# Kernel optimization log

Measured on AMD Instinct MI355X. Metric: run time of the kernel, lower is better.

## Reference

```python
import jax, jax.numpy as jnp
import numpy as np

N = 16384      # nodes (256 chess boards x 64 squares)
E = 393216     # edges (avg degree 24)
G = 256        # graphs
HID = 128
H = 4
C = 32         # head dim
L = 8          # 4 blocks x 2 GATv2Conv
NODE_DIM = 21
EDGE_DIM = 6


def setup_inputs() -> dict:
    key = jax.random.key(0)
    ks = jax.random.split(key, 12)
    x = jax.random.normal(ks[0], (N, NODE_DIM), jnp.float32)
    edge_index = jax.random.randint(ks[1], (2, E), 0, N, dtype=jnp.int32)
    edge_attr = jax.random.uniform(ks[2], (E, EDGE_DIM), dtype=jnp.float32)
    batch = jnp.sort(jax.random.randint(ks[3], (N,), 0, G, dtype=jnp.int32))

    def w(k, shape, fan_in):
        return jax.random.normal(k, shape, jnp.float32) * (1.0 / np.sqrt(fan_in))

    Win = w(ks[4], (NODE_DIM, HID), NODE_DIM)
    b_in = jnp.zeros((HID,), jnp.float32)
    Wl = w(ks[5], (L, HID, HID), HID)
    bl = jnp.zeros((L, HID), jnp.float32)
    Wr = w(ks[6], (L, HID, HID), HID)
    br = jnp.zeros((L, HID), jnp.float32)
    We = w(ks[7], (L, EDGE_DIM, HID), EDGE_DIM)
    att = w(ks[8], (L, H, C), C)
    bconv = jnp.zeros((L, HID), jnp.float32)
    gamma = jnp.ones((L, HID), jnp.float32)
    beta = jnp.zeros((L, HID), jnp.float32)
    W1 = w(ks[9], (HID, 64), HID)
    b1 = jnp.zeros((64,), jnp.float32)
    W2 = w(ks[10], (64, 3), 64)
    b2 = jnp.zeros((3,), jnp.float32)
    return dict(x=x, edge_index=edge_index, edge_attr=edge_attr, batch=batch,
                Win=Win, b_in=b_in, Wl=Wl, bl=bl, Wr=Wr, br=br, We=We, att=att,
                bconv=bconv, gamma=gamma, beta=beta, W1=W1, b1=b1, W2=W2, b2=b2)


def _gatv2(h, src, dst, ea, Wl, bl, Wr, br, We, att, bias):
    # PyG GATv2Conv: message j->i uses x_j from lin_l, x_i from lin_r
    xl = (h @ Wl + bl).reshape(N, H, C)
    xr = (h @ Wr + br).reshape(N, H, C)
    ee = (ea @ We).reshape(-1, H, C)
    m = jax.nn.leaky_relu(xl[src] + xr[dst] + ee, 0.2)   # [Ef, H, C]
    s = jnp.einsum('ehc,hc->eh', m, att)                 # [Ef, H]
    smax = jax.ops.segment_max(s, dst, num_segments=N)   # self-loops => no empty segs
    ex = jnp.exp(s - smax[dst])
    den = jax.ops.segment_sum(ex, dst, num_segments=N)
    alpha = ex / den[dst]                                # edge softmax per target node
    out = jax.ops.segment_sum(alpha[:, :, None] * xl[src], dst, num_segments=N)
    return out.reshape(N, HID) + bias


def _bn(x, g, b):
    mu = jnp.mean(x, axis=0)
    var = jnp.var(x, axis=0)
    return g * (x - mu) * jax.lax.rsqrt(var + 1e-5) + b


def reference(x, edge_index, edge_attr, batch, Win, b_in, Wl, bl, Wr, br, We, att,
              bconv, gamma, beta, W1, b1, W2, b2):
    src0, dst0 = edge_index[0], edge_index[1]
    # add self-loops with fill_value='mean' (per-target mean of incoming edge_attr)
    deg = jax.ops.segment_sum(jnp.ones((E,), jnp.float32), dst0, num_segments=N)
    loop_attr = jax.ops.segment_sum(edge_attr, dst0, num_segments=N) / jnp.maximum(deg, 1.0)[:, None]
    idx = jnp.arange(N, dtype=src0.dtype)
    src = jnp.concatenate([src0, idx])
    dst = jnp.concatenate([dst0, idx])
    ea = jnp.concatenate([edge_attr, loop_attr], axis=0)

    h = jax.nn.relu(x @ Win + b_in)
    for blk in range(4):
        res = h
        l = 2 * blk
        h = jax.nn.relu(_bn(_gatv2(h, src, dst, ea, Wl[l], bl[l], Wr[l], br[l], We[l], att[l], bconv[l]), gamma[l], beta[l]))
        l = 2 * blk + 1
        h = _bn(_gatv2(h, src, dst, ea, Wl[l], bl[l], Wr[l], br[l], We[l], att[l], bconv[l]), gamma[l], beta[l])
        h = jax.nn.relu(h + res)

    cnt = jnp.maximum(jax.ops.segment_sum(jnp.ones((N,), jnp.float32), batch, num_segments=G), 1.0)
    pooled = jax.ops.segment_sum(h, batch, num_segments=G) / cnt[:, None]
    logits = jax.nn.relu(pooled @ W1 + b1) @ W2 + b2
    return logits
```

## Files before the change

### kernel.cpp

```cpp
#include <hip/hip_runtime.h>
#include <hip/hip_fp16.h>
#include <math.h>

constexpr int N   = 16384;
constexpr int E   = 393216;
constexpr int G   = 256;
constexpr int HID = 128;
constexpr int SLOT = 64;

__device__ __forceinline__ float red16(float x) {
    union fi { float f; int i; };
    fi a, b;
    a.f = x;
    b.i = __builtin_amdgcn_mov_dpp(a.i, 0x121, 0xf, 0xf, false); a.f += b.f;
    b.i = __builtin_amdgcn_mov_dpp(a.i, 0x122, 0xf, 0xf, false); a.f += b.f;
    b.i = __builtin_amdgcn_mov_dpp(a.i, 0x124, 0xf, 0xf, false); a.f += b.f;
    b.i = __builtin_amdgcn_mov_dpp(a.i, 0x128, 0xf, 0xf, false); a.f += b.f;
    return a.f;
}

__global__ __launch_bounds__(256) void k_scatter(const int* __restrict__ src,
                                                 const int* __restrict__ dst,
                                                 int* __restrict__ fill,
                                                 const float* __restrict__ edge_attr,
                                                 int* __restrict__ csr_src,
                                                 float* __restrict__ csr_ea) {
    int e = blockIdx.x * 256 + threadIdx.x;
    if (e >= E) return;
    int d = dst[e];
    int pos = atomicAdd(&fill[d], 1);
    if (pos > 62) return;
    size_t base = (size_t)d * SLOT + pos;
    csr_src[base] = src[e];
    const float* s = edge_attr + (size_t)e * 6;
    float4 a = {s[0], s[1], s[2], s[3]};
    float4 b = {s[4], s[5], 0.0f, 0.0f};
    float4* dstp = (float4*)(csr_ea + base * 8);
    dstp[0] = a;
    dstp[1] = b;
}

__global__ __launch_bounds__(256) void k_loopattr2(const int* __restrict__ fill,
                                                   int* __restrict__ csr_src,
                                                   float* __restrict__ csr_ea) {
    int i = blockIdx.x * 256 + threadIdx.x;
    if (i >= N) return;
    int deg = fill[i];
    deg = deg > 62 ? 62 : deg;
    size_t e0 = (size_t)i * SLOT;
    float4 sa = {0, 0, 0, 0};
    float sbx = 0.0f, sby = 0.0f;
    for (int e = 0; e < deg; e++) {
        const float4* p = (const float4*)(csr_ea + (e0 + e) * 8);
        float4 a = p[0];
        float4 b = p[1];
        sa.x += a.x; sa.y += a.y; sa.z += a.z; sa.w += a.w;
        sbx += b.x; sby += b.y;
    }
    float inv = 1.0f / fmaxf((float)deg, 1.0f);
    float4 oa = {sa.x * inv, sa.y * inv, sa.z * inv, sa.w * inv};
    float4 ob = {sbx * inv, sby * inv, 0.0f, 0.0f};
    float4* q = (float4*)(csr_ea + (e0 + deg) * 8);
    q[0] = oa;
    q[1] = ob;
    csr_src[e0 + deg] = i;
}

__global__ __launch_bounds__(128) void k_ingemm(const float* __restrict__ x,
                                                const float* __restrict__ Win,
                                                const float* __restrict__ b_in,
                                                float* __restrict__ h) {
    __shared__ float xs[21];
    int i = blockIdx.x;
    int c = threadIdx.x;
    if (c < 21) xs[c] = x[i * 21 + c];
    __syncthreads();
    float acc = b_in[c];
#pragma unroll
    for (int d = 0; d < 21; d++) acc += xs[d] * Win[d * HID + c];
    h[i * HID + c] = fmaxf(acc, 0.0f);
}

__global__ __launch_bounds__(256) void k_gemm_lr(const float* __restrict__ h,
                                                 const float* __restrict__ bns,
                                                 const float* __restrict__ gamma,
                                                 const float* __restrict__ beta,
                                                 float* __restrict__ res,
                                                 const float* __restrict__ Wl,
                                                 const float* __restrict__ bl,
                                                 const float* __restrict__ Wr,
                                                 const float* __restrict__ br,
                                                 __half2* __restrict__ XLh,
                                                 float* __restrict__ XR) {
    __shared__ float hs[16][HID];
    __shared__ float sc[HID], sh[HID];
    int t = threadIdx.x;
    int r0 = blockIdx.x * 16;
    if (bns) {
        if (t < 128) {
            const float invN = 1.0f / (float)N;
            float mean = bns[t] * invN;
            float var  = bns[128 + t] * invN - mean * mean;
            float inv  = rsqrtf(var + 1e-5f);
            float s = gamma[t] * inv;
            sc[t] = s;
            sh[t] = beta[t] - mean * s;
        }
        __syncthreads();
    }
    {
        int row = t >> 4;
        int col = (t & 15) * 8;
        size_t base = (size_t)(r0 + row) * HID + col;
        const float4* src = (const float4*)&h[base];
        float4 a = src[0];
        float4 b = src[1];
        if (bns) {
            float4 s0 = *(const float4*)&sc[col];
            float4 s1 = *(const float4*)&sc[col + 4];
            float4 h0 = *(const float4*)&sh[col];
            float4 h1 = *(const float4*)&sh[col + 4];
            a.x = fmaf(a.x, s0.x, h0.x);
            a.y = fmaf(a.y, s0.y, h0.y);
            a.z = fmaf(a.z, s0.z, h0.z);
            a.w = fmaf(a.w, s0.w, h0.w);
            b.x = fmaf(b.x, s1.x, h1.x);
            b.y = fmaf(b.y, s1.y, h1.y);
            b.z = fmaf(b.z, s1.z, h1.z);
            b.w = fmaf(b.w, s1.w, h1.w);
            if (res) {
                const float4* rp = (const float4*)&res[base];
                float4 ra = rp[0];
                float4 rb = rp[1];
                a.x += ra.x; a.y += ra.y; a.z += ra.z; a.w += ra.w;
                b.x += rb.x; b.y += rb.y; b.z += rb.z; b.w += rb.w;
            }
            a.x = fmaxf(a.x, 0.0f); a.y = fmaxf(a.y, 0.0f);
            a.z = fmaxf(a.z, 0.0f); a.w = fmaxf(a.w, 0.0f);
            b.x = fmaxf(b.x, 0.0f); b.y = fmaxf(b.y, 0.0f);
            b.z = fmaxf(b.z, 0.0f); b.w = fmaxf(b.w, 0.0f);
            if (res) {
                float4* wp = (float4*)&res[base];
                wp[0] = a;
                wp[1] = b;
            }
        }
        float4* dst = (float4*)&hs[row][col];
        dst[0] = a;
        dst[1] = b;
    }
    __syncthreads();
    bool right = t >= 128;
    int cp = (t & 63) * 2;
    int rbase = ((t >> 6) & 1) * 8;
    const float* W    = right ? Wr : Wl;
    const float* bias = right ? br : bl;
    float b0 = bias[cp], b1 = bias[cp + 1];
    float acc0[8], acc1[8];
#pragma unroll
    for (int r = 0; r < 8; r++) { acc0[r] = b0; acc1[r] = b1; }
    for (int k = 0; k < HID; k += 4) {
        float4 h4[8];
#pragma unroll
        for (int r = 0; r < 8; r++) h4[r] = *(const float4*)&hs[rbase + r][k];
#pragma unroll
        for (int kk = 0; kk < 4; kk++) {
            float2 w = *(const float2*)&W[(size_t)(k + kk) * HID + cp];
#pragma unroll
            for (int r = 0; r < 8; r++) {
                float hv = ((const float*)&h4[r])[kk];
                acc0[r] = fmaf(hv, w.x, acc0[r]);
                acc1[r] = fmaf(hv, w.y, acc1[r]);
            }
        }
    }
    if (right) {
#pragma unroll
        for (int r = 0; r < 8; r++) {
            float2 o = {acc0[r], acc1[r]};
            *(float2*)&XR[(size_t)(r0 + rbase + r) * HID + cp] = o;
        }
    } else {
#pragma unroll
        for (int r = 0; r < 8; r++) {
            XLh[(size_t)(r0 + rbase + r) * 64 + (cp >> 1)] =
                __floats2half2_rn(acc0[r], acc1[r]);
        }
    }
}

__global__ __launch_bounds__(256, 4) void k_edge(const int* __restrict__ fill,
                                                 const int* __restrict__ csr_src,
                                                 const float* __restrict__ csr_ea,
                                                 const __half2* __restrict__ xlh,
                                                 const float* __restrict__ xr,
                                                 const float* __restrict__ We_l,
                                                 const float* __restrict__ att_l,
                                                 float* __restrict__ gout) {
    int iv = (blockIdx.x * 256 + threadIdx.x) >> 6;
    int i = __builtin_amdgcn_readfirstlane(iv);
    int lane = threadIdx.x & 63;
    int hh = lane >> 4;
    int ss = lane & 15;
    int ch0 = hh * 32 + 2 * ss;

    const float LOG2E = 1.44269504088896f;
    float a0 = att_l[ch0] * LOG2E, a1 = att_l[ch0 + 1] * LOG2E;
    float we0[6], we1[6];
#pragma unroll
    for (int d = 0; d < 6; d++) {
        float2 wv = *(const float2*)&We_l[d * HID + ch0];
        we0[d] = wv.x;
        we1[d] = wv.y;
    }

    float2 xr2 = *(const float2*)&xr[(size_t)i * HID + ch0];
    float rd = 0.0f, acc0 = 0.0f, acc1 = 0.0f;
    int deg = __builtin_amdgcn_readfirstlane(fill[i]);
    deg = deg > 62 ? 62 : deg;
    int e0 = i * SLOT;
    int e1 = e0 + deg + 1;
    int nedge = deg + 1;
    int nfull = nedge >> 2;
    int efull = e0 + (nfull << 2);

    auto ld_idx = [&](int e, int out[4]) {
#pragma unroll
        for (int k = 0; k < 4; k++) {
            int ec = e + k;
            ec = (ec < e1) ? ec : (e1 - 1);
            out[k] = __builtin_amdgcn_readfirstlane(csr_src[ec]);
        }
    };
    auto ld_xl = [&](const int idx[4], __half2 out[4]) {
#pragma unroll
        for (int k = 0; k < 4; k++)
            out[k] = xlh[(size_t)idx[k] * 64 + lane];
    };
    auto ld_ea = [&](int e, float4 outA[4], float2 outB[4]) {
#pragma unroll
        for (int k = 0; k < 4; k++) {
            const float* p = csr_ea + (size_t)(e + k) * 8;
            outA[k] = *(const float4*)p;
            outB[k] = *(const float2*)(p + 4);
        }
    };
    auto bodyF = [&](const __half2 xlv[4], const float4 eA[4], const float2 eB[4]) {
#pragma unroll
        for (int k = 0; k < 4; k++) {
            float2 xf = __half22float2(xlv[k]);
            float u0 = eA[k].x * we0[0], u1 = eA[k].x * we1[0];
            u0 = fmaf(eA[k].y, we0[1], u0); u1 = fmaf(eA[k].y, we1[1], u1);
            u0 = fmaf(eA[k].z, we0[2], u0); u1 = fmaf(eA[k].z, we1[2], u1);
            u0 = fmaf(eA[k].w, we0[3], u0); u1 = fmaf(eA[k].w, we1[3], u1);
            u0 = fmaf(eB[k].x, we0[4], u0); u1 = fmaf(eB[k].x, we1[4], u1);
            u0 = fmaf(eB[k].y, we0[5], u0); u1 = fmaf(eB[k].y, we1[5], u1);
            float m0 = xf.x + xr2.x + u0;
            float m1 = xf.y + xr2.y + u1;
            m0 = fmaxf(m0, 0.2f * m0);
            m1 = fmaxf(m1, 0.2f * m1);
            float pv = m0 * a0;
            pv = fmaf(m1, a1, pv);
            pv = red16(pv);
            float ex = exp2f(pv);
            rd += ex;
            acc0 = fmaf(ex, xf.x, acc0);
            acc1 = fmaf(ex, xf.y, acc1);
        }
    };

    int iA[4], iB[4];
    __half2 x0[4], x1[4];
    float4 A0[4], A1[4];
    float2 B0[4], B1[4];
    ld_idx(e0, iA);
    ld_idx(e0 + 4, iB);
    ld_xl(iA, x0);
    ld_ea(e0, A0, B0);
    int e = e0, nf = nfull;
    while (nf >= 2) {
        ld_idx(e + 8, iA);
        ld_xl(iB, x1);
        ld_ea(e + 4, A1, B1);
        bodyF(x0, A0, B0);
        ld_idx(e + 12, iB);
        ld_xl(iA, x0);
        ld_ea(e + 8, A0, B0);
        bodyF(x1, A1, B1);
        e += 8; nf -= 2;
    }
    if (nf == 1) {
        bodyF(x0, A0, B0);
    }
    int rem = nedge & 3;
    if (rem) {
        int it[4];
        __half2 xt[4];
        ld_idx(efull, it);
        ld_xl(it, xt);
#pragma unroll
        for (int k = 0; k < 4; k++) {
            int ee = efull + k;
            int ec = (ee < e1) ? ee : (e1 - 1);
            const float* p = csr_ea + (size_t)ec * 8;
            float4 eaA = *(const float4*)p;
            float2 eaB = *(const float2*)(p + 4);
            float2 xf = __half22float2(xt[k]);
            float u0 = eaA.x * we0[0], u1 = eaA.x * we1[0];
            u0 = fmaf(eaA.y, we0[1], u0); u1 = fmaf(eaA.y, we1[1], u1);
            u0 = fmaf(eaA.z, we0[2], u0); u1 = fmaf(eaA.z, we1[2], u1);
            u0 = fmaf(eaA.w, we0[3], u0); u1 = fmaf(eaA.w, we1[3], u1);
            u0 = fmaf(eaB.x, we0[4], u0); u1 = fmaf(eaB.x, we1[4], u1);
            u0 = fmaf(eaB.y, we0[5], u0); u1 = fmaf(eaB.y, we1[5], u1);
            float m0 = xf.x + xr2.x + u0;
            float m1 = xf.y + xr2.y + u1;
            m0 = fmaxf(m0, 0.2f * m0);
            m1 = fmaxf(m1, 0.2f * m1);
            float pv = m0 * a0;
            pv = fmaf(m1, a1, pv);
            pv = red16(pv);
            pv = (ee < e1) ? pv : -INFINITY;
            float ex = exp2f(pv);
            rd += ex;
            acc0 = fmaf(ex, xf.x, acc0);
            acc1 = fmaf(ex, xf.y, acc1);
        }
    }
    float inv = 1.0f / rd;
    float2 o = {acc0 * inv, acc1 * inv};
    *(float2*)&gout[(size_t)i * HID + ch0] = o;
}

__global__ __launch_bounds__(256) void k_bnstats(const float* __restrict__ v,
                                                 float* __restrict__ sums) {
    __shared__ float l_s[256], l_q[256];
    int t = threadIdx.x;
    int c = t & 127;
    int half = t >> 7;
    int r = blockIdx.x * 64 + half;
    float s = 0.0f, q = 0.0f;
    for (int it = 0; it < 32; it++, r += 2) {
        float val = v[(size_t)r * HID + c];
        s += val;
        q = fmaf(val, val, q);
    }
    l_s[t] = s; l_q[t] = q;
    __syncthreads();
    if (t < 128) {
        s = l_s[t] + l_s[t + 128];
        atomicAdd(&sums[c], s);
    } else {
        q = l_q[t] + l_q[t - 128];
        atomicAdd(&sums[128 + c], q);
    }
}

__global__ __launch_bounds__(128) void k_pool(const float* __restrict__ gout,
                                              const float* __restrict__ res,
                                              const float* __restrict__ bns,
                                              const float* __restrict__ gamma,
                                              const float* __restrict__ beta,
                                              const int* __restrict__ batch,
                                              const float* __restrict__ W1,
                                              const float* __restrict__ b1,
                                              const float* __restrict__ W2,
                                              const float* __restrict__ b2,
                                              float* __restrict__ out) {
    __shared__ float pooled[HID];
    __shared__ float hid[64];
    __shared__ int bounds[2];
    int g = blockIdx.x;
    int t = threadIdx.x;
    if (t < 2) {
        int target = g + t;
        int lo = 0, hi = N;
        while (lo < hi) {
            int mid = (lo + hi) >> 1;
            if (batch[mid] < target) lo = mid + 1; else hi = mid;
        }
        bounds[t] = lo;
    }
    const float invN = 1.0f / (float)N;
    float mean = bns[t] * invN;
    float var  = bns[128 + t] * invN - mean * mean;
    float scb  = gamma[t] * rsqrtf(var + 1e-5f);
    float shb  = beta[t] - mean * scb;
    __syncthreads();
    int s = bounds[0], e = bounds[1];
    float acc = 0.0f;
    for (int r = s; r < e; r++) {
        float v = fmaf(gout[(size_t)r * HID + t], scb, shb) + res[(size_t)r * HID + t];
        acc += fmaxf(v, 0.0f);
    }
    float cntf = fmaxf((float)(e - s), 1.0f);
    pooled[t] = acc / cntf;
    __syncthreads();
    if (t < 64) {
        float a = b1[t];
#pragma unroll 4
        for (int c = 0; c < HID; c++) a += pooled[c] * W1[c * 64 + t];
        hid[t] = fmaxf(a, 0.0f);
    }
    __syncthreads();
    if (t < 3) {
        float a = b2[t];
#pragma unroll
        for (int j = 0; j < 64; j++) a += hid[j] * W2[j * 3 + t];
        out[g * 3 + t] = a;
    }
}

extern "C" void kernel_launch(void* const* d_in, const int* in_sizes, int n_in,
                              void* d_out, int out_size, void* d_ws, size_t ws_size,
                              hipStream_t stream) {
    const float* x         = (const float*)d_in[0];
    const int*   edge_index= (const int*)d_in[1];
    const float* edge_attr = (const float*)d_in[2];
    const int*   batch     = (const int*)d_in[3];
    const float* Win       = (const float*)d_in[4];
    const float* b_in      = (const float*)d_in[5];
    const float* Wl        = (const float*)d_in[6];
    const float* bl        = (const float*)d_in[7];
    const float* Wr        = (const float*)d_in[8];
    const float* br        = (const float*)d_in[9];
    const float* We        = (const float*)d_in[10];
    const float* att       = (const float*)d_in[11];
    const float* gamma     = (const float*)d_in[13];
    const float* beta      = (const float*)d_in[14];
    const float* W1        = (const float*)d_in[15];
    const float* b1        = (const float*)d_in[16];
    const float* W2        = (const float*)d_in[17];
    const float* b2        = (const float*)d_in[18];
    float* out = (float*)d_out;

    const int* src0 = edge_index;
    const int* dst0 = edge_index + E;

    char* ws = (char*)d_ws;
    size_t off = 0;
    auto alloc = [&](size_t bytes) -> void* {
        void* p = ws + off;
        off += (bytes + 255) & ~(size_t)255;
        return p;
    };
    int*     fill      = (int*)alloc((size_t)N * sizeof(int));
    float*   bnsums    = (float*)alloc((size_t)8 * 256 * sizeof(float));
    int*     csr_src   = (int*)alloc((size_t)N * SLOT * sizeof(int));
    float*   csr_ea    = (float*)alloc((size_t)N * SLOT * 8 * sizeof(float) + 512);
    float*   H0        = (float*)alloc((size_t)N * HID * sizeof(float));
    __half2* XLh       = (__half2*)alloc((size_t)N * 64 * sizeof(__half2));
    float*   XR        = (float*)alloc((size_t)N * HID * sizeof(float));
    float*   GOUT      = (float*)alloc((size_t)N * HID * sizeof(float));

    size_t zbytes = (size_t)N * sizeof(int) + 8 * 256 * sizeof(float);
    hipMemsetAsync(fill, 0, zbytes, stream);
    k_scatter<<<(E + 255) / 256, 256, 0, stream>>>(src0, dst0, fill,
                                                   edge_attr, csr_src, csr_ea);
    k_loopattr2<<<(N + 255) / 256, 256, 0, stream>>>(fill, csr_src, csr_ea);
    k_ingemm<<<N, 128, 0, stream>>>(x, Win, b_in, H0);

    for (int l = 0; l < 8; l++) {
        bool odd = (l & 1) != 0;
        const float* hin;
        const float* bns_in = nullptr;
        const float* g_in = nullptr;
        const float* b_in2 = nullptr;
        float* res = nullptr;
        if (l == 0) {
            hin = H0;
        } else {
            hin = GOUT;
            bns_in = bnsums + (l - 1) * 256;
            g_in  = gamma + (size_t)(l - 1) * HID;
            b_in2 = beta  + (size_t)(l - 1) * HID;
            if (!odd) res = H0;
        }
        k_gemm_lr<<<N / 16, 256, 0, stream>>>(hin, bns_in, g_in, b_in2, res,
                                              Wl + (size_t)l * HID * HID, bl + l * HID,
                                              Wr + (size_t)l * HID * HID, br + l * HID,
                                              XLh, XR);
        k_edge<<<N / 4, 256, 0, stream>>>(fill, csr_src, csr_ea,
                                          XLh, XR,
                                          We + (size_t)l * 6 * HID,
                                          att + (size_t)l * HID, GOUT);
        k_bnstats<<<256, 256, 0, stream>>>(GOUT, bnsums + l * 256);
    }
    k_pool<<<G, 128, 0, stream>>>(GOUT, H0, bnsums + 7 * 256,
                                  gamma + 7 * HID, beta + 7 * HID,
                                  batch, W1, b1, W2, b2, out);
}
```

Baseline: 716.1 us.

## Move node linear projections to split-fp16 MFMA with pre-transposed weights

Replaces the scalar FP32 FMA loop in the Wl/Wr projection kernel with 16x16x32 f16 MFMA instructions. Accuracy is kept near fp32 by splitting activations and weights into hi/lo fp16 parts and summing three products. A new kernel converts and transposes the weights once per call, and the projection now handles 32 rows per block. This adds a prep launch and extra MFMA passes, but it targets a GEMM that is only part of a pipeline dominated by the edge kernel.

```diff
diff --git a/kernel.cpp b/kernel.cpp
--- a/kernel.cpp
+++ b/kernel.cpp
@@ -7,6 +7,9 @@
 constexpr int G   = 256;
 constexpr int HID = 128;
 constexpr int SLOT = 64;
+
+typedef _Float16 f16x8 __attribute__((ext_vector_type(8)));
+typedef float    f32x4 __attribute__((ext_vector_type(4)));
 
 __device__ __forceinline__ float red16(float x) {
     union fi { float f; int i; };
@@ -81,21 +84,47 @@
     h[i * HID + c] = fmaxf(acc, 0.0f);
 }
 
+__global__ __launch_bounds__(128) void k_prepw(const float* __restrict__ Wl,
+                                               const float* __restrict__ Wr,
+                                               _Float16* __restrict__ WT) {
+    int b = blockIdx.x;
+    int col = b & 127;
+    int mat = (b >> 7) & 1;
+    int l = b >> 8;
+    int k = threadIdx.x;
+    const float* W = mat ? Wr : Wl;
+    float w = W[((size_t)l * 128 + k) * 128 + col];
+    _Float16 hi = (_Float16)w;
+    _Float16 lo = (_Float16)(w - (float)hi);
+    size_t base = ((size_t)(l * 2 + mat) * 2) << 14;
+    WT[base + (size_t)col * 128 + k] = hi;
+    WT[base + 16384 + (size_t)col * 128 + k] = lo;
+}
+
+#define BN4(V, S, H) { V.x = fmaf(V.x, S.x, H.x); V.y = fmaf(V.y, S.y, H.y); \
+                       V.z = fmaf(V.z, S.z, H.z); V.w = fmaf(V.w, S.w, H.w); }
+#define ADD4(V, R)   { float4 _r = (R); V.x += _r.x; V.y += _r.y; \
+                       V.z += _r.z; V.w += _r.w; }
+#define RELU4(V)     { V.x = fmaxf(V.x, 0.f); V.y = fmaxf(V.y, 0.f); \
+                       V.z = fmaxf(V.z, 0.f); V.w = fmaxf(V.w, 0.f); }
+#define SPLIT(F, HIV, LOV, IDX) { float _f = (F); _Float16 _h = (_Float16)_f; \
+                       HIV[IDX] = _h; LOV[IDX] = (_Float16)(_f - (float)_h); }
+
 __global__ __launch_bounds__(256) void k_gemm_lr(const float* __restrict__ h,
                                                  const float* __restrict__ bns,
                                                  const float* __restrict__ gamma,
                                                  const float* __restrict__ beta,
                                                  float* __restrict__ res,
-                                                 const float* __restrict__ Wl,
+                                                 const _Float16* __restrict__ WT,
                                                  const float* __restrict__ bl,
-                                                 const float* __restrict__ Wr,
                                                  const float* __restrict__ br,
                                                  __half2* __restrict__ XLh,
                                                  float* __restrict__ XR) {
-    __shared__ float hs[16][HID];
+    __shared__ _Float16 hs_hi[32][136];
+    __shared__ _Float16 hs_lo[32][136];
     __shared__ float sc[HID], sh[HID];
     int t = threadIdx.x;
-    int r0 = blockIdx.x * 16;
+    int r0 = blockIdx.x * 32;
     if (bns) {
         if (t < 128) {
             const float invN = 1.0f / (float)N;
@@ -109,82 +138,104 @@
         __syncthreads();
     }
     {
-        int row = t >> 4;
-        int col = (t & 15) * 8;
-        size_t base = (size_t)(r0 + row) * HID + col;
-        const float4* src = (const float4*)&h[base];
-        float4 a = src[0];
-        float4 b = src[1];
+        int row = t >> 3;
+        int cb  = (t & 7) * 16;
+        size_t base = (size_t)(r0 + row) * HID + cb;
+        const float4* srcp = (const float4*)&h[base];
+        float4 v0 = srcp[0], v1 = srcp[1], v2 = srcp[2], v3 = srcp[3];
         if (bns) {
-            float4 s0 = *(const float4*)&sc[col];
-            float4 s1 = *(const float4*)&sc[col + 4];
-            float4 h0 = *(const float4*)&sh[col];
-            float4 h1 = *(const float4*)&sh[col + 4];
-            a.x = fmaf(a.x, s0.x, h0.x);
-            a.y = fmaf(a.y, s0.y, h0.y);
-            a.z = fmaf(a.z, s0.z, h0.z);
-            a.w = fmaf(a.w, s0.w, h0.w);
-            b.x = fmaf(b.x, s1.x, h1.x);
-            b.y = fmaf(b.y, s1.y, h1.y);
-            b.z = fmaf(b.z, s1.z, h1.z);
-            b.w = fmaf(b.w, s1.w, h1.w);
+            float4 s0 = *(const float4*)&sc[cb];
+            float4 s1 = *(const float4*)&sc[cb + 4];
+            float4 s2 = *(const float4*)&sc[cb + 8];
+            float4 s3 = *(const float4*)&sc[cb + 12];
+            float4 h0 = *(const float4*)&sh[cb];
+            float4 h1 = *(const float4*)&sh[cb + 4];
+            float4 h2 = *(const float4*)&sh[cb + 8];
+            float4 h3 = *(const float4*)&sh[cb + 12];
+            BN4(v0, s0, h0); BN4(v1, s1, h1); BN4(v2, s2, h2); BN4(v3, s3, h3);
             if (res) {
                 const float4* rp = (const float4*)&res[base];
-                float4 ra = rp[0];
-                float4 rb = rp[1];
-                a.x += ra.x; a.y += ra.y; a.z += ra.z; a.w += ra.w;
-                b.x += rb.x; b.y += rb.y; b.z += rb.z; b.w += rb.w;
+                ADD4(v0, rp[0]); ADD4(v1, rp[1]); ADD4(v2, rp[2]); ADD4(v3, rp[3]);
             }
-            a.x = fmaxf(a.x, 0.0f); a.y = fmaxf(a.y, 0.0f);
-            a.z = fmaxf(a.z, 0.0f); a.w = fmaxf(a.w, 0.0f);
-            b.x = fmaxf(b.x, 0.0f); b.y = fmaxf(b.y, 0.0f);
-            b.z = fmaxf(b.z, 0.0f); b.w = fmaxf(b.w, 0.0f);
+            RELU4(v0); RELU4(v1); RELU4(v2); RELU4(v3);
             if (res) {
                 float4* wp = (float4*)&res[base];
-                wp[0] = a;
-                wp[1] = b;
+                wp[0] = v0; wp[1] = v1; wp[2] = v2; wp[3] = v3;
             }
         }
-        float4* dst = (float4*)&hs[row][col];
-        dst[0] = a;
-        dst[1] = b;
+        f16x8 hi0, hi1, lo0, lo1;
+        SPLIT(v0.x, hi0, lo0, 0) SPLIT(v0.y, hi0, lo0, 1)
+        SPLIT(v0.z, hi0, lo0, 2) SPLIT(v0.w, hi0, lo0, 3)
+        SPLIT(v1.x, hi0, lo0, 4) SPLIT(v1.y, hi0, lo0, 5)
+        SPLIT(v1.z, hi0, lo0, 6) SPLIT(v1.w, hi0, lo0, 7)
+        SPLIT(v2.x, hi1, lo1, 0) SPLIT(v2.y, hi1, lo1, 1)
+        SPLIT(v2.z, hi1, lo1, 2) SPLIT(v2.w, hi1, lo1, 3)
+        SPLIT(v3.x, hi1, lo1, 4) SPLIT(v3.y, hi1, lo1, 5)
+        SPLIT(v3.z, hi1, lo1, 6) SPLIT(v3.w, hi1, lo1, 7)
+        *(f16x8*)&hs_hi[row][cb]     = hi0;
+        *(f16x8*)&hs_hi[row][cb + 8] = hi1;
+        *(f16x8*)&hs_lo[row][cb]     = lo0;
+        *(f16x8*)&hs_lo[row][cb + 8] = lo1;
     }
     __syncthreads();
-    bool right = t >= 128;
-    int cp = (t & 63) * 2;
-    int rbase = ((t >> 6) & 1) * 8;
-    const float* W    = right ? Wr : Wl;
-    const float* bias = right ? br : bl;
-    float b0 = bias[cp], b1 = bias[cp + 1];
-    float acc0[8], acc1[8];
-#pragma unroll
-    for (int r = 0; r < 8; r++) { acc0[r] = b0; acc1[r] = b1; }
-    for (int k = 0; k < HID; k += 4) {
-        float4 h4[8];
-#pragma unroll
-        for (int r = 0; r < 8; r++) h4[r] = *(const float4*)&hs[rbase + r][k];
-#pragma unroll
-        for (int kk = 0; kk < 4; kk++) {
-            float2 w = *(const float2*)&W[(size_t)(k + kk) * HID + cp];
-#pragma unroll
-            for (int r = 0; r < 8; r++) {
-                float hv = ((const float*)&h4[r])[kk];
-                acc0[r] = fmaf(hv, w.x, acc0[r]);
-                acc1[r] = fmaf(hv, w.y, acc1[r]);
+
+    int wv   = t >> 6;
+    int lane = t & 63;
+    int mat  = wv >> 1;
+    int ch   = wv & 1;
+    int ln15 = lane & 15;
+    int kg   = lane >> 4;
+    const _Float16* Whi = WT + ((size_t)mat * 2) * 16384;
+    const float* bias = mat ? br : bl;
+    f32x4 acc[2][4];
+#pragma unroll
+    for (int c = 0; c < 4; c++) {
+        float bv = bias[(ch * 4 + c) * 16 + ln15];
+        f32x4 b4 = {bv, bv, bv, bv};
+        acc[0][c] = b4;
+        acc[1][c] = b4;
+    }
+#pragma unroll
+    for (int kt = 0; kt < 4; kt++) {
+        int k0 = kt * 32 + kg * 8;
+        f16x8 ahi0 = *(const f16x8*)&hs_hi[ln15][k0];
+        f16x8 ahi1 = *(const f16x8*)&hs_hi[16 + ln15][k0];
+        f16x8 alo0 = *(const f16x8*)&hs_lo[ln15][k0];
+        f16x8 alo1 = *(const f16x8*)&hs_lo[16 + ln15][k0];
+#pragma unroll
+        for (int c = 0; c < 4; c++) {
+            int col = (ch * 4 + c) * 16 + ln15;
+            const _Float16* wp = Whi + (size_t)col * 128 + k0;
+            f16x8 bhi = *(const f16x8*)wp;
+            f16x8 blo = *(const f16x8*)(wp + 16384);
+            acc[0][c] = __builtin_amdgcn_mfma_f32_16x16x32_f16(ahi0, bhi, acc[0][c], 0, 0, 0);
+            acc[1][c] = __builtin_amdgcn_mfma_f32_16x16x32_f16(ahi1, bhi, acc[1][c], 0, 0, 0);
+            acc[0][c] = __builtin_amdgcn_mfma_f32_16x16x32_f16(alo0, bhi, acc[0][c], 0, 0, 0);
+            acc[1][c] = __builtin_amdgcn_mfma_f32_16x16x32_f16(alo1, bhi, acc[1][c], 0, 0, 0);
+            acc[0][c] = __builtin_amdgcn_mfma_f32_16x16x32_f16(ahi0, blo, acc[0][c], 0, 0, 0);
+            acc[1][c] = __builtin_amdgcn_mfma_f32_16x16x32_f16(ahi1, blo, acc[1][c], 0, 0, 0);
+        }
+    }
+#pragma unroll
+    for (int rt = 0; rt < 2; rt++) {
+        int rowb = r0 + rt * 16 + kg * 4;
+#pragma unroll
+        for (int c = 0; c < 4; c++) {
+            int col = (ch * 4 + c) * 16 + ln15;
+            if (mat) {
+#pragma unroll
+                for (int r = 0; r < 4; r++)
+                    XR[(size_t)(rowb + r) * 128 + col] = acc[rt][c][r];
+            } else {
+#pragma unroll
+                for (int r = 0; r < 4; r++) {
+                    float v = acc[rt][c][r];
+                    float w = __shfl_xor(v, 1);
+                    if (!(lane & 1))
+                        XLh[(size_t)(rowb + r) * 64 + (col >> 1)] =
+                            __floats2half2_rn(v, w);
+                }
             }
-        }
-    }
-    if (right) {
-#pragma unroll
-        for (int r = 0; r < 8; r++) {
-            float2 o = {acc0[r], acc1[r]};
-            *(float2*)&XR[(size_t)(r0 + rbase + r) * HID + cp] = o;
-        }
-    } else {
-#pragma unroll
-        for (int r = 0; r < 8; r++) {
-            XLh[(size_t)(r0 + rbase + r) * 64 + (cp >> 1)] =
-                __floats2half2_rn(acc0[r], acc1[r]);
         }
     }
 }
@@ -451,12 +502,14 @@
     __half2* XLh       = (__half2*)alloc((size_t)N * 64 * sizeof(__half2));
     float*   XR        = (float*)alloc((size_t)N * HID * sizeof(float));
     float*   GOUT      = (float*)alloc((size_t)N * HID * sizeof(float));
+    _Float16* WT       = (_Float16*)alloc((size_t)8 * 4 * 16384 * 2);
 
     size_t zbytes = (size_t)N * sizeof(int) + 8 * 256 * sizeof(float);
     hipMemsetAsync(fill, 0, zbytes, stream);
     k_scatter<<<(E + 255) / 256, 256, 0, stream>>>(src0, dst0, fill,
                                                    edge_attr, csr_src, csr_ea);
     k_loopattr2<<<(N + 255) / 256, 256, 0, stream>>>(fill, csr_src, csr_ea);
+    k_prepw<<<8 * 2 * 128, 128, 0, stream>>>(Wl, Wr, WT);
     k_ingemm<<<N, 128, 0, stream>>>(x, Win, b_in, H0);
 
     for (int l = 0; l < 8; l++) {
@@ -475,9 +528,9 @@
             b_in2 = beta  + (size_t)(l - 1) * HID;
             if (!odd) res = H0;
         }
-        k_gemm_lr<<<N / 16, 256, 0, stream>>>(hin, bns_in, g_in, b_in2, res,
-                                              Wl + (size_t)l * HID * HID, bl + l * HID,
-                                              Wr + (size_t)l * HID * HID, br + l * HID,
+        k_gemm_lr<<<N / 32, 256, 0, stream>>>(hin, bns_in, g_in, b_in2, res,
+                                              WT + (size_t)l * 4 * 16384,
+                                              bl + l * HID, br + l * HID,
                                               XLh, XR);
         k_edge<<<N / 4, 256, 0, stream>>>(fill, csr_src, csr_ea,
                                           XLh, XR,
```

Result: faster. 677.4 us (-5.4%).
